# Optimization experiments

Measured on AMD Instinct MI355X. Metric: run time of the kernel, lower is better.

The kernel has to match this reference:

```python
import jax, jax.numpy as jnp
import numpy as np
import math

N_PATCH = 32768
DIM = 512
L_TOK = 64
W_SIZE = 64
STRIDE = 32


def setup_inputs() -> dict:
    key = jax.random.key(0)
    ks = jax.random.split(key, 12)
    d = DIM
    inp = {
        'feats': jax.random.normal(ks[0], (N_PATCH, d), dtype=jnp.float32),
        'coords': jax.random.uniform(ks[1], (N_PATCH, 2), dtype=jnp.float32),
        'mask': jnp.zeros((N_PATCH,), dtype=bool),
        'z': jax.random.normal(ks[2], (L_TOK, d), dtype=jnp.float32),
        'Wq': jax.random.normal(ks[3], (d, d), dtype=jnp.float32) / math.sqrt(d),
        'Wk': jax.random.normal(ks[4], (d, d), dtype=jnp.float32) / math.sqrt(d),
        'Wv': jax.random.normal(ks[5], (d, d), dtype=jnp.float32) / math.sqrt(d),
        'w1': jax.random.normal(ks[6], (d, 2), dtype=jnp.float32) / math.sqrt(2.0),
        'b1': jnp.zeros((d,), dtype=jnp.float32),
        'w2': jax.random.normal(ks[7], (d, d), dtype=jnp.float32) / math.sqrt(d),
        'b2': jnp.zeros((d,), dtype=jnp.float32),
        'Wo': jax.random.normal(ks[8], (d, d), dtype=jnp.float32) / math.sqrt(d),
        'bo': jnp.zeros((d,), dtype=jnp.float32),
    }
    return inp


def _lstcwa(feats, coords, z, Wq, Wk, Wv, w1, b1, w2, b2, Wo, bo):
    # mask is all-False -> feats kept as-is; N divisible by L -> equal segments
    N, D = feats.shape
    L = z.shape[0]
    n = N // L                       # patches per segment
    nwin = -(-n // STRIDE)           # windows per segment (ceil)

    # window offsets within a segment, [nwin, w]; last window truncated via mask
    off = jnp.arange(nwin)[:, None] * STRIDE + jnp.arange(W_SIZE)[None, :]
    valid = off < n                  # [nwin, w]
    idx = jnp.arange(L)[:, None, None] * n + jnp.minimum(off, n - 1)[None]  # [L,nwin,w]

    q = z @ Wq.T                     # [L, D]
    kf = feats @ Wk.T                # [N, D]
    vf = feats @ Wv.T

    k_win = kf[idx]                  # [L, nwin, w, D]
    v_win = vf[idx]
    c_win = coords[idx]              # [L, nwin, w, 2]

    vf32 = valid.astype(feats.dtype)                      # [nwin, w]
    cnt = vf32.sum(-1)                                    # [nwin]
    c_mean = jnp.einsum('lnwc,nw->lnc', c_win, vf32) / cnt[None, :, None]
    delta = (c_win - c_mean[:, :, None, :]) * vf32[None, :, :, None]

    pos = jax.nn.relu(delta @ w1.T + b1) @ w2.T + b2      # [L, nwin, w, D]
    k_win = k_win + pos

    logits = jnp.einsum('ld,lnwd->lnw', q, k_win) / math.sqrt(D)
    logits = jnp.where(valid[None], logits, -1e9)
    attn = jax.nn.softmax(logits, axis=-1)                # [L, nwin, w]

    z_win = jnp.einsum('lnw,lnwd->lnd', attn, v_win)      # [L, nwin, D]
    # return_alpha=False path: z_l_acc / max(1, len(attn_acc)=0) -> SUM over windows
    Z = z_win.sum(1)                                      # [L, D]
    return Z @ Wo.T + bo


def reference(feats, coords, mask, z, Wq, Wk, Wv, w1, b1, w2, b2, Wo, bo):
    # mask is all-False by construction (static shapes under jit)
    return _lstcwa(feats, coords, z, Wq, Wk, Wv, w1, b1, w2, b2, Wo, bo)
```

## Files before the change

kernel.cpp:

```cpp
#include <hip/hip_runtime.h>
#include <math.h>

#define DIMV 512
#define LTOK 64
#define SEG  512
#define NWIN 16
#define WSZ  64
#define INV_SQRT_D 0.044194173824159216f

__device__ __forceinline__ float wave_sum(float v) {
#pragma unroll
  for (int m = 1; m < 64; m <<= 1) v += __shfl_xor(v, m, 64);
  return v;
}
__device__ __forceinline__ float wave_max(float v) {
#pragma unroll
  for (int m = 1; m < 64; m <<= 1) v = fmaxf(v, __shfl_xor(v, m, 64));
  return v;
}

__global__ __launch_bounds__(256, 4) void k_q(const float* __restrict__ z,
    const float* __restrict__ Wq, float* __restrict__ q)
{
  int l = blockIdx.x >> 4, c = blockIdx.x & 15;
  int wave = threadIdx.x >> 6, lane = threadIdx.x & 63;
  int e0 = lane << 3;
  const float* zp = z + l * DIMV + e0;
  float x0[8];
  *(float4*)&x0[0] = *(const float4*)zp;
  *(float4*)&x0[4] = *(const float4*)(zp + 4);
  int d0 = c * 32 + wave * 8;
  float rf[8][8];
#pragma unroll
  for (int k = 0; k < 8; ++k) {
    const float* rp = Wq + (size_t)(d0 + k) * DIMV + e0;
    *(float4*)&rf[k][0] = *(const float4*)rp;
    *(float4*)&rf[k][4] = *(const float4*)(rp + 4);
  }
#pragma unroll
  for (int k = 0; k < 8; ++k) {
    float p = 0.f;
#pragma unroll
    for (int j = 0; j < 8; ++j) p = fmaf(rf[k][j], x0[j], p);
    p = wave_sum(p);
    if (lane == k) q[l * DIMV + d0 + k] = p;
  }
}

__global__ __launch_bounds__(256) void k_qproj(const float* __restrict__ q,
    const float* __restrict__ Wk, const float* __restrict__ w2,
    const float* __restrict__ b2, float* __restrict__ qk,
    float* __restrict__ qw2, float* __restrict__ qb2)
{
  int l = blockIdx.x >> 3, ec = blockIdx.x & 7;
  int wave = threadIdx.x >> 6, lane = threadIdx.x & 63;
  int t = threadIdx.x;
  __shared__ float qs[DIMV];
  __shared__ float pk[4][64], pw[4][64];
  qs[t] = q[l * DIMV + t];
  qs[t + 256] = q[l * DIMV + t + 256];
  __syncthreads();
  int e = ec * 64 + lane;
  int d0 = wave * 128;
  float ak = 0.f, aw = 0.f;
#pragma unroll 8
  for (int dd = 0; dd < 128; ++dd) {
    int d = d0 + dd;
    float qd = qs[d];
    ak = fmaf(qd, Wk[(size_t)d * DIMV + e], ak);
    aw = fmaf(qd, w2[(size_t)d * DIMV + e], aw);
  }
  pk[wave][lane] = ak;
  pw[wave][lane] = aw;
  __syncthreads();
  if (wave == 0) {
    qk[l * DIMV + e] = pk[0][lane] + pk[1][lane] + pk[2][lane] + pk[3][lane];
  } else if (wave == 1) {
    qw2[l * DIMV + e] = pw[0][lane] + pw[1][lane] + pw[2][lane] + pw[3][lane];
  } else if (wave == 2 && ec == 0) {
    int e0 = lane << 3;
    float pb = 0.f;
#pragma unroll
    for (int j = 0; j < 8; ++j) pb = fmaf(qs[e0 + j], b2[e0 + j], pb);
    pb = wave_sum(pb);
    if (lane == 0) qb2[l] = pb;
  }
}

__global__ __launch_bounds__(256, 2) void k_attn(
    const float* __restrict__ feats, const float* __restrict__ coords,
    const float* __restrict__ qk,  const float* __restrict__ qw2,
    const float* __restrict__ qb2, const float* __restrict__ w1,
    const float* __restrict__ b1,  float* __restrict__ upart)
{
  int bid = blockIdx.x;
  int swz = (bid & 7) * 128 + (bid >> 3);
  int l = swz >> 4, n = swz & 15;
  int wave = threadIdx.x >> 6, lane = threadIdx.x & 63;
  int e0 = lane << 3;

  __shared__ float dxs[WSZ], dys[WSZ], lg[WSZ], attnv[WSZ];
  __shared__ float upacc[4][DIMV];

  int base = n * 32;
  int nvalid = SEG - base; if (nvalid > WSZ) nvalid = WSZ;
  const float* fwin = feats + ((size_t)l * SEG + base) * DIMV;

  float rf[16][8];
#pragma unroll
  for (int k = 0; k < 16; ++k) {
    int r = wave * 16 + k;
    if (r < nvalid) {
      const float* rp = fwin + (size_t)r * DIMV + e0;
      *(float4*)&rf[k][0] = *(const float4*)rp;
      *(float4*)&rf[k][4] = *(const float4*)(rp + 4);
    } else {
#pragma unroll
      for (int j = 0; j < 8; ++j) rf[k][j] = 0.f;
    }
  }

  float qk8[8], qw8[8], w1a[8], w1b[8], b18[8];
  {
    const float* p = qk + l * DIMV + e0;
    *(float4*)&qk8[0] = *(const float4*)p;
    *(float4*)&qk8[4] = *(const float4*)(p + 4);
    p = qw2 + l * DIMV + e0;
    *(float4*)&qw8[0] = *(const float4*)p;
    *(float4*)&qw8[4] = *(const float4*)(p + 4);
    float w1v[16];
#pragma unroll
    for (int i = 0; i < 4; ++i) *(float4*)&w1v[i * 4] = *(const float4*)(w1 + e0 * 2 + i * 4);
#pragma unroll
    for (int j = 0; j < 8; ++j) { w1a[j] = w1v[2 * j]; w1b[j] = w1v[2 * j + 1]; }
    p = b1 + e0;
    *(float4*)&b18[0] = *(const float4*)p;
    *(float4*)&b18[4] = *(const float4*)(p + 4);
  }
  float qb2l = qb2[l];

  if (wave == 0) {
    bool v = lane < nvalid;
    float cx = 0.f, cy = 0.f;
    if (v) {
      const float* cp = coords + ((size_t)(l * SEG + base + lane)) * 2;
      cx = cp[0]; cy = cp[1];
    }
    float inv = 1.0f / (float)nvalid;
    float mx = wave_sum(cx) * inv;
    float my = wave_sum(cy) * inv;
    dxs[lane] = v ? cx - mx : 0.f;
    dys[lane] = v ? cy - my : 0.f;
  }
  __syncthreads();

#pragma unroll
  for (int k = 0; k < 16; ++k) {
    int r = wave * 16 + k;
    float dx = dxs[r], dy = dys[r];
    float p = 0.f;
#pragma unroll
    for (int j = 0; j < 8; ++j) {
      float h = fmaf(dx, w1a[j], fmaf(dy, w1b[j], b18[j]));
      p = fmaf(fmaxf(h, 0.f), qw8[j], p);
      p = fmaf(qk8[j], rf[k][j], p);
    }
    p = wave_sum(p);
    if (lane == k) lg[r] = (r < nvalid) ? (p + qb2l) * INV_SQRT_D : -1e9f;
  }
  __syncthreads();

  if (wave == 0) {
    float v = lg[lane];
    float m = wave_max(v);
    float ex = __expf(v - m);
    float s = wave_sum(ex);
    attnv[lane] = ex / s;
  }
  __syncthreads();

  float u8[8];
#pragma unroll
  for (int j = 0; j < 8; ++j) u8[j] = 0.f;
#pragma unroll
  for (int k = 0; k < 16; ++k) {
    float a = attnv[wave * 16 + k];
#pragma unroll
    for (int j = 0; j < 8; ++j) u8[j] = fmaf(a, rf[k][j], u8[j]);
  }
  *(float4*)&upacc[wave][e0]     = *(float4*)&u8[0];
  *(float4*)&upacc[wave][e0 + 4] = *(float4*)&u8[4];
  __syncthreads();
  int t = threadIdx.x;
#pragma unroll
  for (int i = 0; i < 2; ++i) {
    int e = t + 256 * i;
    upart[((size_t)(l * NWIN) + n) * DIMV + e] =
        upacc[0][e] + upacc[1][e] + upacc[2][e] + upacc[3][e];
  }
}

__global__ __launch_bounds__(512) void k_ured(const float* __restrict__ upart,
    float* __restrict__ U)
{
  int l = blockIdx.x, t = threadIdx.x;
  float a = 0.f;
#pragma unroll
  for (int n = 0; n < NWIN; ++n) a += upart[((size_t)(l * NWIN) + n) * DIMV + t];
  U[l * DIMV + t] = a;
}

__global__ __launch_bounds__(256, 4) void k_uv(const float* __restrict__ U,
    const float* __restrict__ Wv, float* __restrict__ tbuf)
{
  int l = blockIdx.x >> 4, c = blockIdx.x & 15;
  int wave = threadIdx.x >> 6, lane = threadIdx.x & 63;
  int e0 = lane << 3;
  const float* up = U + l * DIMV + e0;
  float x0[8];
  *(float4*)&x0[0] = *(const float4*)up;
  *(float4*)&x0[4] = *(const float4*)(up + 4);
  int f0 = c * 32 + wave * 8;
  float rf[8][8];
#pragma unroll
  for (int k = 0; k < 8; ++k) {
    const float* rp = Wv + (size_t)(f0 + k) * DIMV + e0;
    *(float4*)&rf[k][0] = *(const float4*)rp;
    *(float4*)&rf[k][4] = *(const float4*)(rp + 4);
  }
#pragma unroll
  for (int k = 0; k < 8; ++k) {
    float p = 0.f;
#pragma unroll
    for (int j = 0; j < 8; ++j) p = fmaf(rf[k][j], x0[j], p);
    p = wave_sum(p);
    if (lane == k) tbuf[l * DIMV + f0 + k] = p;
  }
}

__global__ __launch_bounds__(256, 4) void k_out(const float* __restrict__ tbuf,
    const float* __restrict__ Wo, const float* __restrict__ bo,
    float* __restrict__ out)
{
  int l = blockIdx.x >> 4, c = blockIdx.x & 15;
  int wave = threadIdx.x >> 6, lane = threadIdx.x & 63;
  int e0 = lane << 3;
  const float* tp = tbuf + l * DIMV + e0;
  float x0[8];
  *(float4*)&x0[0] = *(const float4*)tp;
  *(float4*)&x0[4] = *(const float4*)(tp + 4);
  int d0 = c * 32 + wave * 8;
  float rf[8][8];
#pragma unroll
  for (int k = 0; k < 8; ++k) {
    const float* rp = Wo + (size_t)(d0 + k) * DIMV + e0;
    *(float4*)&rf[k][0] = *(const float4*)rp;
    *(float4*)&rf[k][4] = *(const float4*)(rp + 4);
  }
#pragma unroll
  for (int k = 0; k < 8; ++k) {
    float p = 0.f;
#pragma unroll
    for (int j = 0; j < 8; ++j) p = fmaf(rf[k][j], x0[j], p);
    p = wave_sum(p);
    if (lane == k) out[l * DIMV + d0 + k] = p + bo[d0 + k];
  }
}

extern "C" void kernel_launch(void* const* d_in, const int* in_sizes, int n_in,
                              void* d_out, int out_size, void* d_ws, size_t ws_size,
                              hipStream_t stream) {
  (void)in_sizes; (void)n_in; (void)out_size; (void)ws_size;
  const float* feats  = (const float*)d_in[0];
  const float* coords = (const float*)d_in[1];
  const float* z   = (const float*)d_in[3];
  const float* Wq  = (const float*)d_in[4];
  const float* Wk  = (const float*)d_in[5];
  const float* Wv  = (const float*)d_in[6];
  const float* w1  = (const float*)d_in[7];
  const float* b1  = (const float*)d_in[8];
  const float* w2  = (const float*)d_in[9];
  const float* b2  = (const float*)d_in[10];
  const float* Wo  = (const float*)d_in[11];
  const float* bo  = (const float*)d_in[12];
  float* out = (float*)d_out;

  float* q     = (float*)d_ws;
  float* qk    = q     + LTOK * DIMV;
  float* qw2   = qk    + LTOK * DIMV;
  float* qb2   = qw2   + LTOK * DIMV;
  float* U     = qb2   + LTOK;
  float* tbuf  = U     + LTOK * DIMV;
  float* upart = tbuf  + LTOK * DIMV;

  hipLaunchKernelGGL(k_q,     dim3(LTOK * 16), dim3(256), 0, stream, z, Wq, q);
  hipLaunchKernelGGL(k_qproj, dim3(LTOK * 8),  dim3(256), 0, stream,
                     q, Wk, w2, b2, qk, qw2, qb2);
  hipLaunchKernelGGL(k_attn,  dim3(LTOK * NWIN), dim3(256), 0, stream,
                     feats, coords, qk, qw2, qb2, w1, b1, upart);
  hipLaunchKernelGGL(k_ured,  dim3(LTOK),      dim3(512), 0, stream, upart, U);
  hipLaunchKernelGGL(k_uv,    dim3(LTOK * 16), dim3(256), 0, stream, U, Wv, tbuf);
  hipLaunchKernelGGL(k_out,   dim3(LTOK * 16), dim3(256), 0, stream, tbuf, Wo, bo, out);
}
```

Baseline: 59.85 us.

## Split window attention into per-patch dot and weighted-sum kernels without overlap reloads

Each block used to load a full 64-row overlapping window, so every feats row was read twice. The attention kernel is now split in two. k_dot computes two logits per patch row, one for each window containing it, using window coordinate means precomputed inside k_q. k_wsum then runs the softmax for the two windows that touch each 32-row chunk and accumulates the combined weights times feats in one pass. Each kernel reads feats once per row, but that is two full passes over feats plus an extra launch and logit buffers in workspace, in exchange for lower register pressure and higher occupancy.

```diff
diff --git a/kernel.cpp b/kernel.cpp
--- a/kernel.cpp
+++ b/kernel.cpp
@@ -20,7 +20,8 @@
 }
 
 __global__ __launch_bounds__(256, 4) void k_q(const float* __restrict__ z,
-    const float* __restrict__ Wq, float* __restrict__ q)
+    const float* __restrict__ Wq, const float* __restrict__ coords,
+    float* __restrict__ q, float* __restrict__ cmean)
 {
   int l = blockIdx.x >> 4, c = blockIdx.x & 15;
   int wave = threadIdx.x >> 6, lane = threadIdx.x & 63;
@@ -44,6 +45,23 @@
     for (int j = 0; j < 8; ++j) p = fmaf(rf[k][j], x0[j], p);
     p = wave_sum(p);
     if (lane == k) q[l * DIMV + d0 + k] = p;
+  }
+  if (wave == 0) {
+    int n = c;
+    int nvalid = (n == 15) ? 32 : 64;
+    bool v = lane < nvalid;
+    float cx = 0.f, cy = 0.f;
+    if (v) {
+      const float* cp = coords + ((size_t)(l * SEG + n * 32 + lane)) * 2;
+      cx = cp[0]; cy = cp[1];
+    }
+    float inv = 1.0f / (float)nvalid;
+    float mx = wave_sum(cx) * inv;
+    float my = wave_sum(cy) * inv;
+    if (lane == 0) {
+      cmean[(l * NWIN + n) * 2]     = mx;
+      cmean[(l * NWIN + n) * 2 + 1] = my;
+    }
   }
 }
 
@@ -87,38 +105,16 @@
   }
 }
 
-__global__ __launch_bounds__(256, 2) void k_attn(
+__global__ __launch_bounds__(256, 4) void k_dot(
     const float* __restrict__ feats, const float* __restrict__ coords,
-    const float* __restrict__ qk,  const float* __restrict__ qw2,
-    const float* __restrict__ qb2, const float* __restrict__ w1,
-    const float* __restrict__ b1,  float* __restrict__ upart)
-{
-  int bid = blockIdx.x;
-  int swz = (bid & 7) * 128 + (bid >> 3);
-  int l = swz >> 4, n = swz & 15;
+    const float* __restrict__ cmean, const float* __restrict__ qk,
+    const float* __restrict__ qw2,  const float* __restrict__ qb2,
+    const float* __restrict__ w1,   const float* __restrict__ b1,
+    float* __restrict__ lgt_hi, float* __restrict__ lgt_lo)
+{
+  int l = blockIdx.x >> 4, c = blockIdx.x & 15;
   int wave = threadIdx.x >> 6, lane = threadIdx.x & 63;
   int e0 = lane << 3;
-
-  __shared__ float dxs[WSZ], dys[WSZ], lg[WSZ], attnv[WSZ];
-  __shared__ float upacc[4][DIMV];
-
-  int base = n * 32;
-  int nvalid = SEG - base; if (nvalid > WSZ) nvalid = WSZ;
-  const float* fwin = feats + ((size_t)l * SEG + base) * DIMV;
-
-  float rf[16][8];
-#pragma unroll
-  for (int k = 0; k < 16; ++k) {
-    int r = wave * 16 + k;
-    if (r < nvalid) {
-      const float* rp = fwin + (size_t)r * DIMV + e0;
-      *(float4*)&rf[k][0] = *(const float4*)rp;
-      *(float4*)&rf[k][4] = *(const float4*)(rp + 4);
-    } else {
-#pragma unroll
-      for (int j = 0; j < 8; ++j) rf[k][j] = 0.f;
-    }
-  }
 
   float qk8[8], qw8[8], w1a[8], w1b[8], b18[8];
   {
@@ -138,64 +134,108 @@
     *(float4*)&b18[4] = *(const float4*)(p + 4);
   }
   float qb2l = qb2[l];
+  int rbase = c * 32 + wave * 8;
+  const float* fbase = feats + ((size_t)l * SEG) * DIMV;
+  const float* cbase = coords + ((size_t)l * SEG) * 2;
+  const float* mbase = cmean + (size_t)l * NWIN * 2;
+
+#pragma unroll
+  for (int batch = 0; batch < 2; ++batch) {
+    int rb = rbase + batch * 4;
+    float rf[4][8];
+#pragma unroll
+    for (int k = 0; k < 4; ++k) {
+      const float* rp = fbase + (size_t)(rb + k) * DIMV + e0;
+      *(float4*)&rf[k][0] = *(const float4*)rp;
+      *(float4*)&rf[k][4] = *(const float4*)(rp + 4);
+    }
+#pragma unroll
+    for (int k = 0; k < 4; ++k) {
+      int r = rb + k;
+      int nh = r >> 5;
+      int nl = nh - 1; int nlc = (nl < 0) ? 0 : nl;
+      float cx = cbase[r * 2], cy = cbase[r * 2 + 1];
+      float dxh = cx - mbase[nh * 2],  dyh = cy - mbase[nh * 2 + 1];
+      float dxl = cx - mbase[nlc * 2], dyl = cy - mbase[nlc * 2 + 1];
+      float pd = 0.f, ph = 0.f, pl = 0.f;
+#pragma unroll
+      for (int j = 0; j < 8; ++j) {
+        pd = fmaf(qk8[j], rf[k][j], pd);
+        float hh = fmaf(dxh, w1a[j], fmaf(dyh, w1b[j], b18[j]));
+        ph = fmaf(fmaxf(hh, 0.f), qw8[j], ph);
+        float hl = fmaf(dxl, w1a[j], fmaf(dyl, w1b[j], b18[j]));
+        pl = fmaf(fmaxf(hl, 0.f), qw8[j], pl);
+      }
+      float sh = wave_sum(pd + ph);
+      float sl = wave_sum(pd + pl);
+      int idx = batch * 4 + k;
+      if (lane == idx) {
+        lgt_hi[l * SEG + r] = (sh + qb2l) * INV_SQRT_D;
+        lgt_lo[l * SEG + r] = (sl + qb2l) * INV_SQRT_D;
+      }
+    }
+  }
+}
+
+__global__ __launch_bounds__(256, 4) void k_wsum(
+    const float* __restrict__ feats, const float* __restrict__ lgt_hi,
+    const float* __restrict__ lgt_lo, float* __restrict__ upart)
+{
+  int l = blockIdx.x >> 4, c = blockIdx.x & 15;
+  int wave = threadIdx.x >> 6, lane = threadIdx.x & 63;
+  int e0 = lane << 3, t = threadIdx.x;
+  __shared__ float att2[2][WSZ];
+  __shared__ float upacc[4][DIMV];
 
   if (wave == 0) {
-    bool v = lane < nvalid;
-    float cx = 0.f, cy = 0.f;
-    if (v) {
-      const float* cp = coords + ((size_t)(l * SEG + base + lane)) * 2;
-      cx = cp[0]; cy = cp[1];
-    }
-    float inv = 1.0f / (float)nvalid;
-    float mx = wave_sum(cx) * inv;
-    float my = wave_sum(cy) * inv;
-    dxs[lane] = v ? cx - mx : 0.f;
-    dys[lane] = v ? cy - my : 0.f;
+    float lg;
+    if (c == 15 && lane >= 32) lg = -1e9f;
+    else {
+      int r = c * 32 + lane;
+      lg = (lane < 32) ? lgt_hi[l * SEG + r] : lgt_lo[l * SEG + r];
+    }
+    float m = wave_max(lg);
+    float ex = __expf(lg - m);
+    float s = wave_sum(ex);
+    att2[0][lane] = ex / s;
+  } else if (wave == 1) {
+    if (c == 0) {
+      att2[1][lane] = 0.f;
+    } else {
+      int r = (c - 1) * 32 + lane;
+      float lg = (lane < 32) ? lgt_hi[l * SEG + r] : lgt_lo[l * SEG + r];
+      float m = wave_max(lg);
+      float ex = __expf(lg - m);
+      float s = wave_sum(ex);
+      att2[1][lane] = ex / s;
+    }
   }
   __syncthreads();
 
-#pragma unroll
-  for (int k = 0; k < 16; ++k) {
-    int r = wave * 16 + k;
-    float dx = dxs[r], dy = dys[r];
-    float p = 0.f;
-#pragma unroll
-    for (int j = 0; j < 8; ++j) {
-      float h = fmaf(dx, w1a[j], fmaf(dy, w1b[j], b18[j]));
-      p = fmaf(fmaxf(h, 0.f), qw8[j], p);
-      p = fmaf(qk8[j], rf[k][j], p);
-    }
-    p = wave_sum(p);
-    if (lane == k) lg[r] = (r < nvalid) ? (p + qb2l) * INV_SQRT_D : -1e9f;
-  }
-  __syncthreads();
-
-  if (wave == 0) {
-    float v = lg[lane];
-    float m = wave_max(v);
-    float ex = __expf(v - m);
-    float s = wave_sum(ex);
-    attnv[lane] = ex / s;
-  }
-  __syncthreads();
-
+  int rbase = c * 32 + wave * 8;
+  const float* fbase = feats + ((size_t)l * SEG) * DIMV;
   float u8[8];
 #pragma unroll
   for (int j = 0; j < 8; ++j) u8[j] = 0.f;
 #pragma unroll
-  for (int k = 0; k < 16; ++k) {
-    float a = attnv[wave * 16 + k];
-#pragma unroll
-    for (int j = 0; j < 8; ++j) u8[j] = fmaf(a, rf[k][j], u8[j]);
+  for (int k = 0; k < 8; ++k) {
+    int r = rbase + k;
+    int j31 = r & 31;
+    float g = att2[0][j31] + att2[1][32 + j31];
+    const float* rp = fbase + (size_t)r * DIMV + e0;
+    float f8[8];
+    *(float4*)&f8[0] = *(const float4*)rp;
+    *(float4*)&f8[4] = *(const float4*)(rp + 4);
+#pragma unroll
+    for (int j = 0; j < 8; ++j) u8[j] = fmaf(g, f8[j], u8[j]);
   }
   *(float4*)&upacc[wave][e0]     = *(float4*)&u8[0];
   *(float4*)&upacc[wave][e0 + 4] = *(float4*)&u8[4];
   __syncthreads();
-  int t = threadIdx.x;
 #pragma unroll
   for (int i = 0; i < 2; ++i) {
     int e = t + 256 * i;
-    upart[((size_t)(l * NWIN) + n) * DIMV + e] =
+    upart[((size_t)(l * NWIN) + c) * DIMV + e] =
         upacc[0][e] + upacc[1][e] + upacc[2][e] + upacc[3][e];
   }
 }
@@ -289,16 +329,22 @@
   float* qk    = q     + LTOK * DIMV;
   float* qw2   = qk    + LTOK * DIMV;
   float* qb2   = qw2   + LTOK * DIMV;
-  float* U     = qb2   + LTOK;
+  float* cmean = qb2   + LTOK;
+  float* lgh   = cmean + LTOK * NWIN * 2;
+  float* lgl   = lgh   + LTOK * SEG;
+  float* U     = lgl   + LTOK * SEG;
   float* tbuf  = U     + LTOK * DIMV;
   float* upart = tbuf  + LTOK * DIMV;
 
-  hipLaunchKernelGGL(k_q,     dim3(LTOK * 16), dim3(256), 0, stream, z, Wq, q);
-  hipLaunchKernelGGL(k_qproj, dim3(LTOK * 8),  dim3(256), 0, stream,
+  hipLaunchKernelGGL(k_q,     dim3(LTOK * NWIN), dim3(256), 0, stream,
+                     z, Wq, coords, q, cmean);
+  hipLaunchKernelGGL(k_qproj, dim3(LTOK * 8),    dim3(256), 0, stream,
                      q, Wk, w2, b2, qk, qw2, qb2);
-  hipLaunchKernelGGL(k_attn,  dim3(LTOK * NWIN), dim3(256), 0, stream,
-                     feats, coords, qk, qw2, qb2, w1, b1, upart);
-  hipLaunchKernelGGL(k_ured,  dim3(LTOK),      dim3(512), 0, stream, upart, U);
-  hipLaunchKernelGGL(k_uv,    dim3(LTOK * 16), dim3(256), 0, stream, U, Wv, tbuf);
-  hipLaunchKernelGGL(k_out,   dim3(LTOK * 16), dim3(256), 0, stream, tbuf, Wo, bo, out);
-}
+  hipLaunchKernelGGL(k_dot,   dim3(LTOK * NWIN), dim3(256), 0, stream,
+                     feats, coords, cmean, qk, qw2, qb2, w1, b1, lgh, lgl);
+  hipLaunchKernelGGL(k_wsum,  dim3(LTOK * NWIN), dim3(256), 0, stream,
+                     feats, lgh, lgl, upart);
+  hipLaunchKernelGGL(k_ured,  dim3(LTOK),        dim3(512), 0, stream, upart, U);
+  hipLaunchKernelGGL(k_uv,    dim3(LTOK * NWIN), dim3(256), 0, stream, U, Wv, tbuf);
+  hipLaunchKernelGGL(k_out,   dim3(LTOK * NWIN), dim3(256), 0, stream, tbuf, Wo, bo, out);
+}
```

Result: slower. 65.05 us (+8.7%).
